# Kernel optimization log

Hardware: AMD Instinct MI355X
Metric: run time of the kernel (lower is better)

## Reference

```python
import jax, jax.numpy as jnp
import numpy as np

DIV_COEF = 1.0
EPS = 1e-8  # torch.cosine_similarity default eps


def setup_inputs() -> dict:
    key = jax.random.key(0)
    id_ = jax.random.normal(key, (8192, 512), dtype=jnp.float32)
    return {"id": id_}


def reference(id):
    # cosine similarity via norm + GEMM (math identical to broadcast form)
    norms = jnp.linalg.norm(id, axis=1)                      # [N]
    dots = id @ id.T                                          # [N, N]
    sim = dots / jnp.maximum(norms[:, None] * norms[None, :], EPS)
    n = id.shape[0]
    # zero diagonal, clamp negatives to zero, mean over full NxN
    off_diag = 1.0 - jnp.eye(n, dtype=sim.dtype)
    id_sim = off_diag * sim
    l_id_div = jnp.mean(jnp.where(id_sim < 0, 0.0, id_sim))
    total_loss = DIV_COEF * l_id_div
    return (total_loss, l_id_div)
```

## Files before the change

kernel.cpp:

```cpp
#include <hip/hip_runtime.h>
#include <stdint.h>

#define NROWS 8192
#define KDIM  512
#define BM    128
#define BK    256
#define NKI   (KDIM / BK)
#define NT    (NROWS / BM)
#define NBLK  (NT * (NT + 1) / 2)

typedef __attribute__((ext_vector_type(4))) float f32x4;
typedef long i64;

__device__ __forceinline__ void async_copy16(const unsigned char* g, unsigned char* l) {
  __builtin_amdgcn_global_load_lds(
      (const __attribute__((address_space(1))) unsigned int*)g,
      (__attribute__((address_space(3))) unsigned int*)l,
      16, 0, 0);
}

__global__ __launch_bounds__(256) void prep_kernel(
    const float* __restrict__ src, unsigned char* __restrict__ dst,
    float* __restrict__ acc) {
  const int row  = blockIdx.x * 4 + (threadIdx.x >> 6);
  const int lane = threadIdx.x & 63;
  const float4 v0 = ((const float4*)src)[row * 128 + lane * 2];
  const float4 v1 = ((const float4*)src)[row * 128 + lane * 2 + 1];
  float ss = v0.x * v0.x + v0.y * v0.y + v0.z * v0.z + v0.w * v0.w
           + v1.x * v1.x + v1.y * v1.y + v1.z * v1.z + v1.w * v1.w;
  #pragma unroll
  for (int off = 32; off > 0; off >>= 1) ss += __shfl_down(ss, off);
  const float rn = 1.0f / sqrtf(__shfl(ss, 0));
  if (row == 0 && lane == 0) *acc = 0.0f;
  int pk0 = __builtin_amdgcn_cvt_pk_fp8_f32(v0.x * rn, v0.y * rn, 0, false);
  pk0     = __builtin_amdgcn_cvt_pk_fp8_f32(v0.z * rn, v0.w * rn, pk0, true);
  int pk1 = __builtin_amdgcn_cvt_pk_fp8_f32(v1.x * rn, v1.y * rn, 0, false);
  pk1     = __builtin_amdgcn_cvt_pk_fp8_f32(v1.z * rn, v1.w * rn, pk1, true);
  const int cg = lane >> 1;
  const int win = cg >> 4;
  const int p  = (cg & 15) ^ (row & 15);
  const int hf = (lane & 1) ^ ((row >> 3) & 1);
  uint2 o; o.x = (unsigned int)pk0; o.y = (unsigned int)pk1;
  ((uint2*)dst)[row * 64 + win * 32 + p * 2 + hf] = o;
}

__device__ __forceinline__ int tri_base(int b) {
  return b * NT - (b * (b - 1)) / 2;
}

__global__ __launch_bounds__(256) void sim_reduce_kernel(
    const unsigned char* __restrict__ idn, float* __restrict__ acc) {
  const int idx = blockIdx.x;
  const float Af = 2.0f * NT + 1.0f;
  int bi = (int)((Af - sqrtf(Af * Af - 8.0f * (float)idx)) * 0.5f);
  while (bi > 0 && tri_base(bi) > idx) bi--;
  while (tri_base(bi + 1) <= idx) bi++;
  const int bj = bi + (idx - tri_base(bi));

  __shared__ __align__(16) unsigned char As[BM * BK];
  __shared__ __align__(16) unsigned char Bs[BM * BK];

  const int tid  = threadIdx.x;
  const int lane = tid & 63;
  const int w    = tid >> 6;
  const int wr   = (w >> 1) * 64;
  const int wc   = (w & 1) * 64;
  const int q    = lane >> 4;
  const int r16  = lane & 15;
  const int hq   = (((q & 1) ^ ((r16 >> 3) & 1))) * 8;

  f32x4 acc_f[4][4];
  #pragma unroll
  for (int i = 0; i < 4; i++)
    #pragma unroll
    for (int j = 0; j < 4; j++)
      acc_f[i][j] = (f32x4){0.f, 0.f, 0.f, 0.f};

  const unsigned char* gA = idn + (size_t)(bi * BM + (tid >> 4)) * KDIM + (tid & 15) * 16;
  const unsigned char* gB = idn + (size_t)(bj * BM + (tid >> 4)) * KDIM + (tid & 15) * 16;
  unsigned char* lA = As + tid * 16;
  unsigned char* lB = Bs + tid * 16;

  #pragma unroll
  for (int t = 0; t < NKI; ++t) {
    if (t) __syncthreads();
    const int ko = t * BK;
    #pragma unroll
    for (int i = 0; i < 8; i++) async_copy16(gA + ko + i * 8192, lA + i * 4096);
    #pragma unroll
    for (int i = 0; i < 8; i++) async_copy16(gB + ko + i * 8192, lB + i * 4096);
    asm volatile("s_waitcnt vmcnt(0)" ::: "memory");
    __syncthreads();

    #pragma unroll
    for (int s = 0; s < 8; s++) {
      const int pos = ((2 * s + (q >> 1)) ^ r16) * 16 + hq;
      i64 a[4], b[4];
      #pragma unroll
      for (int mi = 0; mi < 4; mi++) {
        a[mi] = *(const i64*)&As[(wr + mi * 16 + r16) * BK + pos];
        b[mi] = *(const i64*)&Bs[(wc + mi * 16 + r16) * BK + pos];
      }
      #pragma unroll
      for (int mi = 0; mi < 4; mi++)
        #pragma unroll
        for (int ni = 0; ni < 4; ni++)
          acc_f[mi][ni] = __builtin_amdgcn_mfma_f32_16x16x32_fp8_fp8(
              a[mi], b[ni], acc_f[mi][ni], 0, 0, 0);
    }
  }

  float local = 0.f;
  const bool diag = (bi == bj);
  #pragma unroll
  for (int mi = 0; mi < 4; mi++)
    #pragma unroll
    for (int ni = 0; ni < 4; ni++)
      #pragma unroll
      for (int rr = 0; rr < 4; rr++) {
        const int ri = wr + mi * 16 + q * 4 + rr;
        const int ci = wc + ni * 16 + r16;
        float v = fmaxf(acc_f[mi][ni][rr], 0.f);
        if (diag && ri == ci) v = 0.f;
        local += v;
      }

  #pragma unroll
  for (int off = 32; off > 0; off >>= 1) local += __shfl_down(local, off);
  __syncthreads();
  float* red = (float*)As;
  if (lane == 0) red[w] = local;
  __syncthreads();
  if (tid == 0) {
    float s = red[0] + red[1] + red[2] + red[3];
    if (!diag) s *= 2.f;
    atomicAdd(acc, s);
  }
}

__global__ void finalize_kernel(const float* __restrict__ acc, float* __restrict__ out) {
  const float m = *acc * (1.0f / ((float)NROWS * (float)NROWS));
  out[0] = m;
  out[1] = m;
}

extern "C" void kernel_launch(void* const* d_in, const int* in_sizes, int n_in,
                              void* d_out, int out_size, void* d_ws, size_t ws_size,
                              hipStream_t stream) {
  const float* id = (const float*)d_in[0];
  float* out = (float*)d_out;
  unsigned char* idn = (unsigned char*)d_ws;
  float* acc = (float*)((char*)d_ws + (size_t)NROWS * KDIM);

  prep_kernel<<<NROWS / 4, 256, 0, stream>>>(id, idn, acc);
  sim_reduce_kernel<<<NBLK, 256, 0, stream>>>(idn, acc);
  finalize_kernel<<<1, 1, 0, stream>>>(acc, out);
}
```

Before: 100.5 us.

## Double-buffer LDS tiles with BK=128 to overlap global loads and MFMA

Halves the K tile to 128 and adds two LDS buffers, so the next tile's async global-to-LDS copies are issued while MFMAs run on the current tile, using partial vmcnt waits and raw s_barrier. The prep kernel's fp8 swizzle is changed to match the 128-byte row layout. This targets the exposed load latency of the earlier load-everything-then-compute loop. In exchange there are more loop iterations and barriers, and correctness now depends on the hand-written vmcnt counts and barrier placement.

```diff
diff --git a/kernel.cpp b/kernel.cpp
--- a/kernel.cpp
+++ b/kernel.cpp
@@ -4,7 +4,7 @@
 #define NROWS 8192
 #define KDIM  512
 #define BM    128
-#define BK    256
+#define BK    128
 #define NKI   (KDIM / BK)
 #define NT    (NROWS / BM)
 #define NBLK  (NT * (NT + 1) / 2)
@@ -36,12 +36,12 @@
   pk0     = __builtin_amdgcn_cvt_pk_fp8_f32(v0.z * rn, v0.w * rn, pk0, true);
   int pk1 = __builtin_amdgcn_cvt_pk_fp8_f32(v1.x * rn, v1.y * rn, 0, false);
   pk1     = __builtin_amdgcn_cvt_pk_fp8_f32(v1.z * rn, v1.w * rn, pk1, true);
-  const int cg = lane >> 1;
-  const int win = cg >> 4;
-  const int p  = (cg & 15) ^ (row & 15);
-  const int hf = (lane & 1) ^ ((row >> 3) & 1);
+  const int cg  = lane >> 1;
+  const int win = cg >> 3;
+  const int p   = (cg & 7) ^ (row & 7);
+  const int hf  = (lane & 1) ^ ((row >> 3) & 1);
   uint2 o; o.x = (unsigned int)pk0; o.y = (unsigned int)pk1;
-  ((uint2*)dst)[row * 64 + win * 32 + p * 2 + hf] = o;
+  ((uint2*)dst)[row * 64 + win * 16 + p * 2 + hf] = o;
 }
 
 __device__ __forceinline__ int tri_base(int b) {
@@ -57,8 +57,8 @@
   while (tri_base(bi + 1) <= idx) bi++;
   const int bj = bi + (idx - tri_base(bi));
 
-  __shared__ __align__(16) unsigned char As[BM * BK];
-  __shared__ __align__(16) unsigned char Bs[BM * BK];
+  __shared__ __align__(16) unsigned char As[2][BM * BK];
+  __shared__ __align__(16) unsigned char Bs[2][BM * BK];
 
   const int tid  = threadIdx.x;
   const int lane = tid & 63;
@@ -67,7 +67,8 @@
   const int wc   = (w & 1) * 64;
   const int q    = lane >> 4;
   const int r16  = lane & 15;
-  const int hq   = (((q & 1) ^ ((r16 >> 3) & 1))) * 8;
+  const int rx   = r16 & 7;
+  const int hq   = ((q & 1) ^ ((r16 >> 3) & 1)) * 8;
 
   f32x4 acc_f[4][4];
   #pragma unroll
@@ -76,30 +77,41 @@
     for (int j = 0; j < 4; j++)
       acc_f[i][j] = (f32x4){0.f, 0.f, 0.f, 0.f};
 
-  const unsigned char* gA = idn + (size_t)(bi * BM + (tid >> 4)) * KDIM + (tid & 15) * 16;
-  const unsigned char* gB = idn + (size_t)(bj * BM + (tid >> 4)) * KDIM + (tid & 15) * 16;
-  unsigned char* lA = As + tid * 16;
-  unsigned char* lB = Bs + tid * 16;
+  const unsigned char* gA = idn + (size_t)(bi * BM + (tid >> 3)) * KDIM + (tid & 7) * 16;
+  const unsigned char* gB = idn + (size_t)(bj * BM + (tid >> 3)) * KDIM + (tid & 7) * 16;
+  const int ldso = tid * 16;
+
+  #pragma unroll
+  for (int i = 0; i < 4; i++) async_copy16(gA + (size_t)i * 16384, &As[0][ldso + i * 4096]);
+  #pragma unroll
+  for (int i = 0; i < 4; i++) async_copy16(gB + (size_t)i * 16384, &Bs[0][ldso + i * 4096]);
 
   #pragma unroll
   for (int t = 0; t < NKI; ++t) {
-    if (t) __syncthreads();
-    const int ko = t * BK;
-    #pragma unroll
-    for (int i = 0; i < 8; i++) async_copy16(gA + ko + i * 8192, lA + i * 4096);
-    #pragma unroll
-    for (int i = 0; i < 8; i++) async_copy16(gB + ko + i * 8192, lB + i * 4096);
-    asm volatile("s_waitcnt vmcnt(0)" ::: "memory");
-    __syncthreads();
+    const int cs = t & 1;
+    if (t + 1 < NKI) {
+      const int ns = cs ^ 1;
+      const int ko = (t + 1) * BK;
+      #pragma unroll
+      for (int i = 0; i < 4; i++)
+        async_copy16(gA + ko + (size_t)i * 16384, &As[ns][ldso + i * 4096]);
+      #pragma unroll
+      for (int i = 0; i < 4; i++)
+        async_copy16(gB + ko + (size_t)i * 16384, &Bs[ns][ldso + i * 4096]);
+      asm volatile("s_waitcnt vmcnt(8)" ::: "memory");
+    } else {
+      asm volatile("s_waitcnt vmcnt(0)" ::: "memory");
+    }
+    asm volatile("s_barrier" ::: "memory");
 
     #pragma unroll
-    for (int s = 0; s < 8; s++) {
-      const int pos = ((2 * s + (q >> 1)) ^ r16) * 16 + hq;
+    for (int s = 0; s < 4; s++) {
+      const int pos = ((2 * s + (q >> 1)) ^ rx) * 16 + hq;
       i64 a[4], b[4];
       #pragma unroll
       for (int mi = 0; mi < 4; mi++) {
-        a[mi] = *(const i64*)&As[(wr + mi * 16 + r16) * BK + pos];
-        b[mi] = *(const i64*)&Bs[(wc + mi * 16 + r16) * BK + pos];
+        a[mi] = *(const i64*)&As[cs][(wr + mi * 16 + r16) * BK + pos];
+        b[mi] = *(const i64*)&Bs[cs][(wc + mi * 16 + r16) * BK + pos];
       }
       #pragma unroll
       for (int mi = 0; mi < 4; mi++)
@@ -108,6 +120,8 @@
           acc_f[mi][ni] = __builtin_amdgcn_mfma_f32_16x16x32_fp8_fp8(
               a[mi], b[ni], acc_f[mi][ni], 0, 0, 0);
     }
+
+    asm volatile("s_barrier" ::: "memory");
   }
 
   float local = 0.f;
```

Measured after the change: 98.13 us. 2.3% less time.
